# Kernel optimization log

Hardware: AMD Instinct MI355X
Metric: run time of the kernel (lower is better)

## Reference

```python
import jax, jax.numpy as jnp
import numpy as np

B, S, D, H = 1, 2048, 768, 12
WIN = 128            # window_size
HALF = WIN // 2      # 64
WN = WIN + 1         # each position attends to [i-64, i+64] inclusive -> 129 keys
DH = D // H


def setup_inputs() -> dict:
    key = jax.random.key(0)
    ks = jax.random.split(key, 8)
    scale = 0.02
    return {
        "query": jax.random.normal(ks[0], (B, S, D), dtype=jnp.float32),
        "key":   jax.random.normal(ks[1], (B, S, D), dtype=jnp.float32),
        "value": jax.random.normal(ks[2], (B, S, D), dtype=jnp.float32),
        "Wq": jax.random.normal(ks[3], (D, D), dtype=jnp.float32) * scale,
        "bq": jnp.zeros((D,), dtype=jnp.float32),
        "Wk": jax.random.normal(ks[4], (D, D), dtype=jnp.float32) * scale,
        "bk": jnp.zeros((D,), dtype=jnp.float32),
        "Wv": jax.random.normal(ks[5], (D, D), dtype=jnp.float32) * scale,
        "bv": jnp.zeros((D,), dtype=jnp.float32),
        "Wo": jax.random.normal(ks[6], (D, D), dtype=jnp.float32) * scale,
        "bo": jnp.zeros((D,), dtype=jnp.float32),
    }


def reference(query, key, value, Wq, bq, Wk, bk, Wv, bv, Wo, bo):
    b, s, d = query.shape
    # Linear projections, split heads: [B,S,H,DH]
    q = (query @ Wq + bq).reshape(b, s, H, DH)
    k = (key   @ Wk + bk).reshape(b, s, H, DH)
    v = (value @ Wv + bv).reshape(b, s, H, DH)

    # Window gather indices: pos[i, j] = i - HALF + j, j in [0, WN)
    pos = jnp.arange(s)[:, None] + (jnp.arange(WN)[None, :] - HALF)  # [S, WN]
    valid = (pos >= 0) & (pos < s)                                   # [S, WN]
    idx = jnp.clip(pos, 0, s - 1)

    kw = k[:, idx]  # [B, S, WN, H, DH]
    vw = v[:, idx]  # [B, S, WN, H, DH]

    scores = jnp.einsum('bshd,bswhd->bhsw', q, kw) / np.sqrt(DH)     # [B,H,S,WN]
    scores = jnp.where(valid[None, None, :, :], scores, -jnp.inf)
    attn = jax.nn.softmax(scores, axis=-1)

    ctx = jnp.einsum('bhsw,bswhd->bshd', attn, vw).reshape(b, s, d)  # [B,S,D]
    return ctx @ Wo + bo
```

## Files before the change

### kernel.cpp

```cpp
#include <hip/hip_runtime.h>
#include <math.h>

#define S_LEN 2048
#define DM 768
#define NHEAD 12
#define DHEAD 64
#define HALF_W 64

typedef _Float16 half8 __attribute__((ext_vector_type(8)));
typedef _Float16 half4_t __attribute__((ext_vector_type(4)));
typedef float floatx4 __attribute__((ext_vector_type(4)));

typedef const __attribute__((address_space(1))) unsigned int* gas_ptr;
typedef __attribute__((address_space(3))) unsigned int* las_ptr;
__device__ __forceinline__ void gld_lds16(const void* g, void* l) {
  __builtin_amdgcn_global_load_lds((gas_ptr)g, (las_ptr)l, 16, 0, 0);
}

__global__ __launch_bounds__(256)
void prep_w_kernel(const float* __restrict__ Wq, const float* __restrict__ Wk,
                   const float* __restrict__ Wv, const float* __restrict__ Wo,
                   _Float16* __restrict__ Tq, _Float16* __restrict__ Tk,
                   _Float16* __restrict__ Tv, _Float16* __restrict__ To) {
  __shared__ float t[64][65];
  int b = blockIdx.x;
  int z = b / 144, rem = b % 144;
  const float* W = z == 0 ? Wq : z == 1 ? Wk : z == 2 ? Wv : Wo;
  _Float16* T = z == 0 ? Tq : z == 1 ? Tk : z == 2 ? Tv : To;
  int n0 = (rem % 12) * 64, k0 = (rem / 12) * 64;
  int tx = threadIdx.x & 15, ty = threadIdx.x >> 4;
#pragma unroll
  for (int i = 0; i < 4; ++i) {
    int row = ty + i * 16;
    float4 v = *(const float4*)(W + (size_t)(k0 + row) * DM + n0 + tx * 4);
    t[row][tx * 4 + 0] = v.x; t[row][tx * 4 + 1] = v.y;
    t[row][tx * 4 + 2] = v.z; t[row][tx * 4 + 3] = v.w;
  }
  __syncthreads();
#pragma unroll
  for (int i = 0; i < 4; ++i) {
    int nn = ty + i * 16, kk = tx * 4;
    half4_t h = {(_Float16)t[kk + 0][nn], (_Float16)t[kk + 1][nn],
                 (_Float16)t[kk + 2][nn], (_Float16)t[kk + 3][nn]};
    *(half4_t*)(T + (size_t)(n0 + nn) * DM + k0 + kk) = h;
  }
}

#define GBM 64
#define GBN 64
#define GBK 64
#define ACH 17

__global__ __launch_bounds__(256, 6)
void gemm_qkv_kernel(const float* __restrict__ A0, const float* __restrict__ A1,
                     const float* __restrict__ A2, const _Float16* __restrict__ W0,
                     const _Float16* __restrict__ W1, const _Float16* __restrict__ W2,
                     const float* __restrict__ b0, const float* __restrict__ b1,
                     const float* __restrict__ b2, _Float16* __restrict__ Q,
                     _Float16* __restrict__ K, _Float16* __restrict__ Vt) {
  __shared__ __align__(16) float Asf[GBM * ACH * 4];
  __shared__ __align__(16) _Float16 Bs[GBN * GBK];
  const int bid = blockIdx.x;
  const int xcd = bid & 7;
  const int li = bid >> 3;
  const int panel = xcd * 12 + li / 12;
  const int nb = li % 12;
  const int z = panel >> 5;
  const int m0 = (panel & 31) * GBM;
  const int n0 = nb * GBN;
  const float* A = z == 0 ? A0 : z == 1 ? A1 : A2;
  const _Float16* Wt = z == 0 ? W0 : z == 1 ? W1 : W2;
  const float* bias = z == 0 ? b0 : z == 1 ? b1 : b2;

  const int tid = threadIdx.x;
  const int lane = tid & 63;
  const int w = tid >> 6;
  const int lr = lane & 15;
  const int lq = lane >> 4;
  const int wm = w >> 1, wn = w & 1;
  const int wb = tid & 192;

  floatx4 acc[2][2] = {};

  for (int k0 = 0; k0 < DM; k0 += GBK) {
    __syncthreads();
#pragma unroll
    for (int i = 0; i < 5; ++i) {
      if (i < 4 || tid < 64) {
        int s = i * 256 + tid;
        int m = s / ACH, pos = s % ACH;
        int ch = pos < 16 ? pos : 15;
        gld_lds16(A + (size_t)(m0 + m) * DM + k0 + ch * 4, &Asf[(i * 256 + wb) * 4]);
      }
    }
#pragma unroll
    for (int i = 0; i < 2; ++i) {
      int c = i * 256 + tid;
      int n = c >> 3, j = c & 7, jg = j ^ (n & 7);
      gld_lds16(Wt + (size_t)(n0 + n) * DM + k0 + jg * 8, &Bs[(i * 256 + wb) * 8]);
    }
    __syncthreads();

#pragma unroll
    for (int kh = 0; kh < 2; ++kh) {
      half8 af[2], bf[2];
#pragma unroll
      for (int mt = 0; mt < 2; ++mt) {
        int m = wm * 32 + mt * 16 + lr;
        int j0 = kh * 8 + lq * 2;
        float4 f0 = *(const float4*)&Asf[(m * ACH + j0) * 4];
        float4 f1 = *(const float4*)&Asf[(m * ACH + j0 + 1) * 4];
        af[mt] = half8{(_Float16)f0.x, (_Float16)f0.y, (_Float16)f0.z, (_Float16)f0.w,
                       (_Float16)f1.x, (_Float16)f1.y, (_Float16)f1.z, (_Float16)f1.w};
      }
#pragma unroll
      for (int nt = 0; nt < 2; ++nt) {
        int n = wn * 32 + nt * 16 + lr;
        int j = (kh * 4 + lq) ^ (n & 7);
        bf[nt] = *(const half8*)&Bs[n * GBK + j * 8];
      }
#pragma unroll
      for (int mt = 0; mt < 2; ++mt)
#pragma unroll
        for (int nt = 0; nt < 2; ++nt)
          acc[mt][nt] = __builtin_amdgcn_mfma_f32_16x16x32_f16(af[mt], bf[nt], acc[mt][nt], 0, 0, 0);
    }
  }

#pragma unroll
  for (int mt = 0; mt < 2; ++mt) {
    int row0 = m0 + wm * 32 + mt * 16 + lq * 4;
#pragma unroll
    for (int nt = 0; nt < 2; ++nt) {
      int col = n0 + wn * 32 + nt * 16 + lr;
      float bv = bias[col];
      if (z == 2) {
        half4_t o = {(_Float16)(acc[mt][nt][0] + bv), (_Float16)(acc[mt][nt][1] + bv),
                     (_Float16)(acc[mt][nt][2] + bv), (_Float16)(acc[mt][nt][3] + bv)};
        *(half4_t*)(Vt + (size_t)col * S_LEN + row0) = o;
      } else {
        _Float16* H = z == 0 ? Q : K;
#pragma unroll
        for (int rr = 0; rr < 4; ++rr)
          H[(size_t)(row0 + rr) * DM + col] = (_Float16)(acc[mt][nt][rr] + bv);
      }
    }
  }
}

__global__ __launch_bounds__(256, 6)
void gemm_out_kernel(const _Float16* __restrict__ A, const _Float16* __restrict__ Wt,
                     const float* __restrict__ bias, float* __restrict__ C) {
  __shared__ __align__(16) _Float16 As[GBM * GBK];
  __shared__ __align__(16) _Float16 Bs[GBN * GBK];
  const int bid = blockIdx.x;
  const int xcd = bid & 7;
  const int li = bid >> 3;
  const int m0 = (xcd * 4 + li / 12) * GBM;
  const int n0 = (li % 12) * GBN;
  const int tid = threadIdx.x;
  const int lane = tid & 63;
  const int w = tid >> 6;
  const int lr = lane & 15;
  const int lq = lane >> 4;
  const int wm = w >> 1, wn = w & 1;
  const int wb = tid & 192;

  floatx4 acc[2][2] = {};

  for (int k0 = 0; k0 < DM; k0 += GBK) {
    __syncthreads();
#pragma unroll
    for (int i = 0; i < 2; ++i) {
      int c = i * 256 + tid;
      int m = c >> 3, j = c & 7, jg = j ^ (m & 7);
      gld_lds16(A + (size_t)(m0 + m) * DM + k0 + jg * 8, &As[(i * 256 + wb) * 8]);
    }
#pragma unroll
    for (int i = 0; i < 2; ++i) {
      int c = i * 256 + tid;
      int n = c >> 3, j = c & 7, jg = j ^ (n & 7);
      gld_lds16(Wt + (size_t)(n0 + n) * DM + k0 + jg * 8, &Bs[(i * 256 + wb) * 8]);
    }
    __syncthreads();

#pragma unroll
    for (int kh = 0; kh < 2; ++kh) {
      half8 af[2], bf[2];
#pragma unroll
      for (int mt = 0; mt < 2; ++mt) {
        int m = wm * 32 + mt * 16 + lr;
        int j = (kh * 4 + lq) ^ (m & 7);
        af[mt] = *(const half8*)&As[m * GBK + j * 8];
      }
#pragma unroll
      for (int nt = 0; nt < 2; ++nt) {
        int n = wn * 32 + nt * 16 + lr;
        int j = (kh * 4 + lq) ^ (n & 7);
        bf[nt] = *(const half8*)&Bs[n * GBK + j * 8];
      }
#pragma unroll
      for (int mt = 0; mt < 2; ++mt)
#pragma unroll
        for (int nt = 0; nt < 2; ++nt)
          acc[mt][nt] = __builtin_amdgcn_mfma_f32_16x16x32_f16(af[mt], bf[nt], acc[mt][nt], 0, 0, 0);
    }
  }

#pragma unroll
  for (int mt = 0; mt < 2; ++mt) {
    int row0 = m0 + wm * 32 + mt * 16 + lq * 4;
#pragma unroll
    for (int nt = 0; nt < 2; ++nt) {
      int col = n0 + wn * 32 + nt * 16 + lr;
      float bv = bias[col];
#pragma unroll
      for (int rr = 0; rr < 4; ++rr)
        C[(size_t)(row0 + rr) * DM + col] = acc[mt][nt][rr] + bv;
    }
  }
}

#define ATQ 32

__global__ __launch_bounds__(256, 3)
void swattn_mfma_kernel(const _Float16* __restrict__ qh, const _Float16* __restrict__ kh,
                        const _Float16* __restrict__ vt, _Float16* __restrict__ ctx) {
  __shared__ __align__(16) _Float16 Ks[160 * 64];
  __shared__ __align__(16) _Float16 Vs[64 * 168];
  __shared__ __align__(16) _Float16 QP[32 * 168];
  __shared__ float red[4][32];

  const int tid = threadIdx.x;
  const int lane = tid & 63, w = tid >> 6;
  const int lr = lane & 15, lq = lane >> 4;
  const int bid = blockIdx.x;
  const int x = bid & 7, mid = (bid >> 3) & 7, h = bid >> 6;
  const int s0 = (x * 8 + mid) * ATQ;
  const int wb = tid & 192;

  {
    int r = tid >> 3, j = tid & 7, jg = j ^ (r & 7);
    gld_lds16(qh + (size_t)(s0 + r) * DM + h * DHEAD + jg * 8, &QP[wb * 8]);
  }
#pragma unroll
  for (int i = 0; i < 5; ++i) {
    int c = i * 256 + tid;
    int r = c >> 3, j = c & 7, jg = j ^ (r & 7);
    int pos = s0 - HALF_W + r;
    pos = pos < 0 ? 0 : (pos > S_LEN - 1 ? S_LEN - 1 : pos);
    gld_lds16(kh + (size_t)pos * DM + h * DHEAD + jg * 8, &Ks[(i * 256 + wb) * 8]);
  }
#pragma unroll
  for (int i = 0; i < 6; ++i) {
    int c = i * 256 + tid;
    if (c < 1344) {
      int r = c / 21, j = c % 21;
      int cb = s0 - HALF_W + j * 8;
      cb = cb < 0 ? 0 : (cb > S_LEN - 8 ? S_LEN - 8 : cb);
      gld_lds16(vt + (size_t)(h * DHEAD + r) * S_LEN + cb, &Vs[(i * 256 + wb) * 8]);
    }
  }
  __syncthreads();

  const int qt = w & 1, ph = w >> 1;
  floatx4 sc[5];
  {
    half8 aq[2];
#pragma unroll
    for (int k2 = 0; k2 < 2; ++k2) {
      int r = qt * 16 + lr, j = (k2 * 4 + lq) ^ (r & 7);
      aq[k2] = *(const half8*)&QP[r * DHEAD + j * 8];
    }
#pragma unroll
    for (int t = 0; t < 5; ++t) {
      int pt = ph * 5 + t;
      floatx4 a = {};
#pragma unroll
      for (int k2 = 0; k2 < 2; ++k2) {
        int r = pt * 16 + lr, j = (k2 * 4 + lq) ^ (r & 7);
        half8 bk = *(const half8*)&Ks[r * DHEAD + j * 8];
        a = __builtin_amdgcn_mfma_f32_16x16x32_f16(aq[k2], bk, a, 0, 0, 0);
      }
      sc[t] = a;
    }
  }

  const int qbase = qt * 16 + lq * 4;
  float m4[4] = {-1e30f, -1e30f, -1e30f, -1e30f};
#pragma unroll
  for (int t = 0; t < 5; ++t) {
    int p = (ph * 5 + t) * 16 + lr;
    int g = s0 - HALF_W + p;
#pragma unroll
    for (int rr = 0; rr < 4; ++rr) {
      int q = qbase + rr;
      bool ok = (p >= q) && (p <= q + 128) && (g >= 0) && (g < S_LEN);
      float v = ok ? sc[t][rr] * 0.125f : -1e30f;
      sc[t][rr] = v;
      m4[rr] = fmaxf(m4[rr], v);
    }
  }
#pragma unroll
  for (int off = 1; off <= 8; off <<= 1)
#pragma unroll
    for (int rr = 0; rr < 4; ++rr) m4[rr] = fmaxf(m4[rr], __shfl_xor(m4[rr], off, 64));
  if (lr == 0)
#pragma unroll
    for (int rr = 0; rr < 4; ++rr) red[ph][qbase + rr] = m4[rr];
  __syncthreads();

  float ss[4] = {0.f, 0.f, 0.f, 0.f};
  float mm[4];
#pragma unroll
  for (int rr = 0; rr < 4; ++rr)
    mm[rr] = fmaxf(red[0][qbase + rr], red[1][qbase + rr]);
#pragma unroll
  for (int t = 0; t < 5; ++t)
#pragma unroll
    for (int rr = 0; rr < 4; ++rr) {
      float e = __expf(sc[t][rr] - mm[rr]);
      sc[t][rr] = e;
      ss[rr] += e;
    }
#pragma unroll
  for (int off = 1; off <= 8; off <<= 1)
#pragma unroll
    for (int rr = 0; rr < 4; ++rr) ss[rr] += __shfl_xor(ss[rr], off, 64);
  if (lr == 0)
#pragma unroll
    for (int rr = 0; rr < 4; ++rr) red[2 + ph][qbase + rr] = ss[rr];
  __syncthreads();

#pragma unroll
  for (int rr = 0; rr < 4; ++rr) {
    float inv = 1.f / (red[2][qbase + rr] + red[3][qbase + rr]);
#pragma unroll
    for (int t = 0; t < 5; ++t) {
      int p = (ph * 5 + t) * 16 + lr;
      QP[(qbase + rr) * 168 + p] = (_Float16)(sc[t][rr] * inv);
    }
  }
  __syncthreads();

  {
    const int qt2 = w & 1;
    const int dt0 = (w >> 1) * 2;
    floatx4 a0 = {}, a1 = {};
#pragma unroll
    for (int ks = 0; ks < 5; ++ks) {
      half8 ap = *(const half8*)&QP[(qt2 * 16 + lr) * 168 + ks * 32 + lq * 8];
      half8 bv0 = *(const half8*)&Vs[(dt0 * 16 + lr) * 168 + ks * 32 + lq * 8];
      half8 bv1 = *(const half8*)&Vs[((dt0 + 1) * 16 + lr) * 168 + ks * 32 + lq * 8];
      a0 = __builtin_amdgcn_mfma_f32_16x16x32_f16(ap, bv0, a0, 0, 0, 0);
      a1 = __builtin_amdgcn_mfma_f32_16x16x32_f16(ap, bv1, a1, 0, 0, 0);
    }
#pragma unroll
    for (int rr = 0; rr < 4; ++rr) {
      size_t row = (size_t)(s0 + qt2 * 16 + lq * 4 + rr) * DM + h * DHEAD;
      ctx[row + dt0 * 16 + lr] = (_Float16)a0[rr];
      ctx[row + (dt0 + 1) * 16 + lr] = (_Float16)a1[rr];
    }
  }
}

extern "C" void kernel_launch(void* const* d_in, const int* in_sizes, int n_in,
                              void* d_out, int out_size, void* d_ws, size_t ws_size,
                              hipStream_t stream) {
  const float* query = (const float*)d_in[0];
  const float* key   = (const float*)d_in[1];
  const float* value = (const float*)d_in[2];
  const float* Wq = (const float*)d_in[3];
  const float* bq = (const float*)d_in[4];
  const float* Wk = (const float*)d_in[5];
  const float* bk = (const float*)d_in[6];
  const float* Wv = (const float*)d_in[7];
  const float* bv = (const float*)d_in[8];
  const float* Wo = (const float*)d_in[9];
  const float* bo = (const float*)d_in[10];
  float* out = (float*)d_out;

  const size_t nel = (size_t)S_LEN * DM;
  const size_t wel = (size_t)DM * DM;
  _Float16* Wtq = (_Float16*)d_ws;
  _Float16* Wtk = Wtq + wel;
  _Float16* Wtv = Wtk + wel;
  _Float16* Wto = Wtv + wel;
  _Float16* qh = Wto + wel;
  _Float16* khb = qh + nel;
  _Float16* Vtg = khb + nel;
  _Float16* ctxh = Vtg + nel;

  prep_w_kernel<<<dim3(576), 256, 0, stream>>>(Wq, Wk, Wv, Wo, Wtq, Wtk, Wtv, Wto);
  gemm_qkv_kernel<<<dim3(1152), 256, 0, stream>>>(
      query, key, value, Wtq, Wtk, Wtv, bq, bk, bv, qh, khb, Vtg);
  swattn_mfma_kernel<<<dim3((S_LEN / ATQ) * NHEAD), 256, 0, stream>>>(qh, khb, Vtg, ctxh);
  gemm_out_kernel<<<dim3(384), 256, 0, stream>>>(ctxh, Wto, bo, out);
}
```

Baseline: 135.4 us.

## Load GEMM MFMA fragments directly from global memory, dropping LDS staging

Both the QKV projection GEMM and the output GEMM stop staging A and B tiles in shared memory. Each lane now loads its MFMA fragments straight from global memory (through L1/L2) and converts fp32 A to fp16 in registers. This removes the per-iteration barriers and LDS traffic, and the launch bounds drop from 6 to 4 blocks per SM. The cost is that each tile element is fetched by two waves from global/cache instead of once, with less coalesced access and more register pressure.

```diff
diff --git a/kernel.cpp b/kernel.cpp
--- a/kernel.cpp
+++ b/kernel.cpp
@@ -48,18 +48,14 @@
 
 #define GBM 64
 #define GBN 64
-#define GBK 64
-#define ACH 17
-
-__global__ __launch_bounds__(256, 6)
+
+__global__ __launch_bounds__(256, 4)
 void gemm_qkv_kernel(const float* __restrict__ A0, const float* __restrict__ A1,
                      const float* __restrict__ A2, const _Float16* __restrict__ W0,
                      const _Float16* __restrict__ W1, const _Float16* __restrict__ W2,
                      const float* __restrict__ b0, const float* __restrict__ b1,
                      const float* __restrict__ b2, _Float16* __restrict__ Q,
                      _Float16* __restrict__ K, _Float16* __restrict__ Vt) {
-  __shared__ __align__(16) float Asf[GBM * ACH * 4];
-  __shared__ __align__(16) _Float16 Bs[GBN * GBK];
   const int bid = blockIdx.x;
   const int xcd = bid & 7;
   const int li = bid >> 3;
@@ -78,58 +74,42 @@
   const int lr = lane & 15;
   const int lq = lane >> 4;
   const int wm = w >> 1, wn = w & 1;
-  const int wb = tid & 192;
+
+  const float* Abase = A + (size_t)(m0 + wm * 32 + lr) * DM + lq * 8;
+  const _Float16* Bbase = Wt + (size_t)(n0 + wn * 32 + lr) * DM + lq * 8;
 
   floatx4 acc[2][2] = {};
 
-  for (int k0 = 0; k0 < DM; k0 += GBK) {
-    __syncthreads();
-#pragma unroll
-    for (int i = 0; i < 5; ++i) {
-      if (i < 4 || tid < 64) {
-        int s = i * 256 + tid;
-        int m = s / ACH, pos = s % ACH;
-        int ch = pos < 16 ? pos : 15;
-        gld_lds16(A + (size_t)(m0 + m) * DM + k0 + ch * 4, &Asf[(i * 256 + wb) * 4]);
+  for (int k0 = 0; k0 < DM; k0 += 64) {
+    half8 af[2][2], bf[2][2];
+#pragma unroll
+    for (int kh = 0; kh < 2; ++kh)
+#pragma unroll
+      for (int mt = 0; mt < 2; ++mt) {
+        const float* p = Abase + (size_t)mt * 16 * DM + k0 + kh * 32;
+        float4 f0 = *(const float4*)p;
+        float4 f1 = *(const float4*)(p + 4);
+        af[kh][mt] = half8{(_Float16)f0.x, (_Float16)f0.y, (_Float16)f0.z, (_Float16)f0.w,
+                           (_Float16)f1.x, (_Float16)f1.y, (_Float16)f1.z, (_Float16)f1.w};
       }
-    }
-#pragma unroll
-    for (int i = 0; i < 2; ++i) {
-      int c = i * 256 + tid;
-      int n = c >> 3, j = c & 7, jg = j ^ (n & 7);
-      gld_lds16(Wt + (size_t)(n0 + n) * DM + k0 + jg * 8, &Bs[(i * 256 + wb) * 8]);
-    }
-    __syncthreads();
-
-#pragma unroll
-    for (int kh = 0; kh < 2; ++kh) {
-      half8 af[2], bf[2];
-#pragma unroll
-      for (int mt = 0; mt < 2; ++mt) {
-        int m = wm * 32 + mt * 16 + lr;
-        int j0 = kh * 8 + lq * 2;
-        float4 f0 = *(const float4*)&Asf[(m * ACH + j0) * 4];
-        float4 f1 = *(const float4*)&Asf[(m * ACH + j0 + 1) * 4];
-        af[mt] = half8{(_Float16)f0.x, (_Float16)f0.y, (_Float16)f0.z, (_Float16)f0.w,
-                       (_Float16)f1.x, (_Float16)f1.y, (_Float16)f1.z, (_Float16)f1.w};
-      }
-#pragma unroll
-      for (int nt = 0; nt < 2; ++nt) {
-        int n = wn * 32 + nt * 16 + lr;
-        int j = (kh * 4 + lq) ^ (n & 7);
-        bf[nt] = *(const half8*)&Bs[n * GBK + j * 8];
-      }
+#pragma unroll
+    for (int kh = 0; kh < 2; ++kh)
+#pragma unroll
+      for (int nt = 0; nt < 2; ++nt)
+        bf[kh][nt] = *(const half8*)(Bbase + (size_t)nt * 16 * DM + k0 + kh * 32);
+#pragma unroll
+    for (int kh = 0; kh < 2; ++kh)
 #pragma unroll
       for (int mt = 0; mt < 2; ++mt)
 #pragma unroll
         for (int nt = 0; nt < 2; ++nt)
-          acc[mt][nt] = __builtin_amdgcn_mfma_f32_16x16x32_f16(af[mt], bf[nt], acc[mt][nt], 0, 0, 0);
-    }
-  }
-
+          acc[mt][nt] = __builtin_amdgcn_mfma_f32_16x16x32_f16(af[kh][mt], bf[kh][nt], acc[mt][nt], 0, 0, 0);
+  }
+
+  const int lq4 = lq * 4;
 #pragma unroll
   for (int mt = 0; mt < 2; ++mt) {
-    int row0 = m0 + wm * 32 + mt * 16 + lq * 4;
+    int row0 = m0 + wm * 32 + mt * 16 + lq4;
 #pragma unroll
     for (int nt = 0; nt < 2; ++nt) {
       int col = n0 + wn * 32 + nt * 16 + lr;
@@ -148,11 +128,9 @@
   }
 }
 
-__global__ __launch_bounds__(256, 6)
+__global__ __launch_bounds__(256, 4)
 void gemm_out_kernel(const _Float16* __restrict__ A, const _Float16* __restrict__ Wt,
                      const float* __restrict__ bias, float* __restrict__ C) {
-  __shared__ __align__(16) _Float16 As[GBM * GBK];
-  __shared__ __align__(16) _Float16 Bs[GBN * GBK];
   const int bid = blockIdx.x;
   const int xcd = bid & 7;
   const int li = bid >> 3;
@@ -164,47 +142,31 @@
   const int lr = lane & 15;
   const int lq = lane >> 4;
   const int wm = w >> 1, wn = w & 1;
-  const int wb = tid & 192;
+
+  const _Float16* Abase = A + (size_t)(m0 + wm * 32 + lr) * DM + lq * 8;
+  const _Float16* Bbase = Wt + (size_t)(n0 + wn * 32 + lr) * DM + lq * 8;
 
   floatx4 acc[2][2] = {};
 
-  for (int k0 = 0; k0 < DM; k0 += GBK) {
-    __syncthreads();
-#pragma unroll
-    for (int i = 0; i < 2; ++i) {
-      int c = i * 256 + tid;
-      int m = c >> 3, j = c & 7, jg = j ^ (m & 7);
-      gld_lds16(A + (size_t)(m0 + m) * DM + k0 + jg * 8, &As[(i * 256 + wb) * 8]);
-    }
-#pragma unroll
-    for (int i = 0; i < 2; ++i) {
-      int c = i * 256 + tid;
-      int n = c >> 3, j = c & 7, jg = j ^ (n & 7);
-      gld_lds16(Wt + (size_t)(n0 + n) * DM + k0 + jg * 8, &Bs[(i * 256 + wb) * 8]);
-    }
-    __syncthreads();
-
-#pragma unroll
-    for (int kh = 0; kh < 2; ++kh) {
-      half8 af[2], bf[2];
-#pragma unroll
-      for (int mt = 0; mt < 2; ++mt) {
-        int m = wm * 32 + mt * 16 + lr;
-        int j = (kh * 4 + lq) ^ (m & 7);
-        af[mt] = *(const half8*)&As[m * GBK + j * 8];
-      }
-#pragma unroll
-      for (int nt = 0; nt < 2; ++nt) {
-        int n = wn * 32 + nt * 16 + lr;
-        int j = (kh * 4 + lq) ^ (n & 7);
-        bf[nt] = *(const half8*)&Bs[n * GBK + j * 8];
-      }
+  for (int k0 = 0; k0 < DM; k0 += 64) {
+    half8 af[2][2], bf[2][2];
+#pragma unroll
+    for (int kh = 0; kh < 2; ++kh)
 #pragma unroll
       for (int mt = 0; mt < 2; ++mt)
+        af[kh][mt] = *(const half8*)(Abase + (size_t)mt * 16 * DM + k0 + kh * 32);
+#pragma unroll
+    for (int kh = 0; kh < 2; ++kh)
+#pragma unroll
+      for (int nt = 0; nt < 2; ++nt)
+        bf[kh][nt] = *(const half8*)(Bbase + (size_t)nt * 16 * DM + k0 + kh * 32);
+#pragma unroll
+    for (int kh = 0; kh < 2; ++kh)
+#pragma unroll
+      for (int mt = 0; mt < 2; ++mt)
 #pragma unroll
         for (int nt = 0; nt < 2; ++nt)
-          acc[mt][nt] = __builtin_amdgcn_mfma_f32_16x16x32_f16(af[mt], bf[nt], acc[mt][nt], 0, 0, 0);
-    }
+          acc[mt][nt] = __builtin_amdgcn_mfma_f32_16x16x32_f16(af[kh][mt], bf[kh][nt], acc[mt][nt], 0, 0, 0);
   }
 
 #pragma unroll
```

Result: slower. 202.3 us (+49.4%).
